# Optimization experiments

Measured on AMD Instinct MI355X. Metric: run time of the kernel, lower is better.

Reference implementation:

```python
import jax, jax.numpy as jnp
import numpy as np
import math

B, S, E, H = 4, 2048, 1024, 16
D = E // H  # head_dim = 64
ROPE_BASE = 10000.0


def setup_inputs() -> dict:
    key = jax.random.key(0)
    ks = jax.random.split(key, 8)
    wscale = 1.0 / math.sqrt(E)
    inp = {
        "query": jax.random.normal(ks[0], (B, S, E), dtype=jnp.float32),
        "key": jax.random.normal(ks[1], (B, S, E), dtype=jnp.float32),
        "value": jax.random.normal(ks[2], (B, S, E), dtype=jnp.float32),
        "Wq": jax.random.normal(ks[3], (E, E), dtype=jnp.float32) * wscale,
        "Wk": jax.random.normal(ks[4], (E, E), dtype=jnp.float32) * wscale,
        "Wv": jax.random.normal(ks[5], (E, E), dtype=jnp.float32) * wscale,
        "Wo": jax.random.normal(ks[6], (E, E), dtype=jnp.float32) * wscale,
        "positions": jnp.arange(S, dtype=jnp.int64),
        # True = masked (upper triangle -> causal)
        "attn_mask": jnp.triu(jnp.ones((S, S), dtype=bool), k=1),
    }
    return inp


def _apply_rope(x, positions):
    # x: [B, H, S, D]; rotate-half RoPE convention
    half = D // 2
    inv_freq = 1.0 / (ROPE_BASE ** (jnp.arange(0, D, 2, dtype=jnp.float32) / D))  # [D/2]
    ang = positions.astype(jnp.float32)[:, None] * inv_freq[None, :]  # [S, D/2]
    cos = jnp.concatenate([jnp.cos(ang), jnp.cos(ang)], axis=-1)  # [S, D]
    sin = jnp.concatenate([jnp.sin(ang), jnp.sin(ang)], axis=-1)  # [S, D]
    x1, x2 = x[..., :half], x[..., half:]
    rot = jnp.concatenate([-x2, x1], axis=-1)
    return x * cos[None, None] + rot * sin[None, None]


def reference(query, key, value, Wq, Wk, Wv, Wo, positions, attn_mask):
    # projections (no bias, weight layout [out, in] as in set_weights_from_float)
    q = jnp.einsum('bse,oe->bso', query, Wq).reshape(B, S, H, D).transpose(0, 2, 1, 3)
    k = jnp.einsum('bse,oe->bso', key, Wk).reshape(B, S, H, D).transpose(0, 2, 1, 3)
    v = jnp.einsum('bse,oe->bso', value, Wv).reshape(B, S, H, D).transpose(0, 2, 1, 3)
    q = _apply_rope(q, positions)
    k = _apply_rope(k, positions)
    scale = 1.0 / math.sqrt(D)
    scores = jnp.einsum('bhqd,bhkd->bhqk', q, k) * scale  # [B,H,S,S]
    scores = jnp.where(attn_mask[None, None], -jnp.inf, scores)
    weights = jax.nn.softmax(scores, axis=-1)
    out = jnp.einsum('bhqk,bhkd->bhqd', weights, v)  # [B,H,S,D]
    out = out.transpose(0, 2, 1, 3).reshape(B, S, H * D)
    return jnp.einsum('bso,eo->bse', out, Wo)
```

## Files before the change

kernel.cpp:

```cpp
#include <hip/hip_runtime.h>
#include <hip/hip_bf16.h>
#include <math.h>

typedef __bf16 bf16;
typedef __attribute__((ext_vector_type(8))) __bf16 bf16x8;
typedef __attribute__((ext_vector_type(4))) __bf16 bf16x4;
typedef __attribute__((ext_vector_type(4))) float f32x4;
typedef __attribute__((ext_vector_type(16))) float f32x16;
typedef __attribute__((ext_vector_type(4))) unsigned uint4v;

#define MFMA16 __builtin_amdgcn_mfma_f32_16x16x32_bf16
#define MFMA32 __builtin_amdgcn_mfma_f32_32x32x16_bf16

__device__ __forceinline__ void g2l16(const void* g, void* l) {
    __builtin_amdgcn_global_load_lds(
        (const __attribute__((address_space(1))) void*)g,
        (__attribute__((address_space(3))) void*)l, 16, 0, 0);
}

__device__ __forceinline__ bool is_bf16_buf(const void* p) {
    const int lane = threadIdx.x & 63;
    unsigned w = ((const unsigned*)p)[lane];
    unsigned e = (w >> 7) & 0xFF;
    bool pl = (e == 0) || (e >= 80 && e < 134);
    return __popcll(__ballot(pl)) >= 52;
}

__device__ __forceinline__ void stage_f32(bf16* l, const float* g) {
    float4 f0 = ((const float4*)g)[0];
    float4 f1 = ((const float4*)g)[1];
    bf16x8 t;
    t[0] = (bf16)f0.x; t[1] = (bf16)f0.y; t[2] = (bf16)f0.z; t[3] = (bf16)f0.w;
    t[4] = (bf16)f1.x; t[5] = (bf16)f1.y; t[6] = (bf16)f1.z; t[7] = (bf16)f1.w;
    *(bf16x8*)l = t;
}

__device__ __forceinline__ unsigned cvtpk_bf16(float a, float b) {
    unsigned r;
    asm("v_cvt_pk_bf16_f32 %0, %1, %2" : "=v"(r) : "v"(a), "v"(b));
    return r;
}

__global__ __launch_bounds__(256) void convert7(const void* s0, const void* s1,
                                                const void* s2, const void* s3,
                                                const void* s4, const void* s5,
                                                const void* s6,
                                                bf16* __restrict__ dst) {
    const size_t e = ((size_t)blockIdx.x * 256 + threadIdx.x) * 8;
    const void* src; size_t off; bf16* d;
    if (e < 25165824) {
        const int i = (int)(e >> 23);
        src = i == 0 ? s0 : i == 1 ? s1 : s2;
        off = e & 8388607;
        d   = dst + ((size_t)i << 23) + off;
    } else {
        const size_t e2 = e - 25165824;
        const int i = (int)(e2 >> 20);
        src = i == 0 ? s3 : i == 1 ? s4 : i == 2 ? s5 : s6;
        off = e2 & 1048575;
        d   = dst + 25165824 + ((size_t)i << 20) + off;
    }
    if (is_bf16_buf(src)) {
        *(bf16x8*)d = *((const bf16x8*)((const bf16*)src + off));
    } else {
        stage_f32(d, (const float*)src + off);
    }
}

__device__ __forceinline__ void epi_rope(f32x4 acc[4][4], bf16* __restrict__ C,
                                         int m0, int n0, int wm, int wn,
                                         int quad, int l16, float scale) {
    const float kf = 0.41524101186092029f;
    const float inv0 = exp2f(-(float)l16 * kf);
    const float inv1 = exp2f(-(float)(l16 + 16) * kf);
#pragma unroll
    for (int mi = 0; mi < 4; mi++) {
#pragma unroll
        for (int r = 0; r < 4; r++) {
            const int row = m0 + wm + mi * 16 + quad * 4 + r;
            const float pos = (float)(row & 2047);
#pragma unroll
            for (int p = 0; p < 2; p++) {
                float sn, cs;
                __sincosf(pos * (p ? inv1 : inv0), &sn, &cs);
                const float x1 = acc[mi][p][r];
                const float x2 = acc[mi][p + 2][r];
                const int col = n0 + wn + p * 16 + l16;
                C[(size_t)row * 1024 + col]      = (bf16)((x1 * cs - x2 * sn) * scale);
                C[(size_t)row * 1024 + col + 32] = (bf16)((x2 * cs + x1 * sn) * scale);
            }
        }
    }
}

__device__ __forceinline__ void epi_vt(f32x4 acc[4][4], bf16* __restrict__ C,
                                       int m0, int n0, int wm, int wn,
                                       int quad, int l16) {
#pragma unroll
    for (int mi = 0; mi < 4; mi++) {
        const int rbase = m0 + wm + mi * 16 + quad * 4;
#pragma unroll
        for (int ni = 0; ni < 4; ni++) {
            const int col = n0 + wn + ni * 16 + l16;
            bf16x4 t;
#pragma unroll
            for (int r = 0; r < 4; r++) t[r] = (bf16)acc[mi][ni][r];
            *(bf16x4*)&C[(size_t)col * 8192 + rbase] = t;
        }
    }
}

__device__ __forceinline__ void gemm_core(const bf16* __restrict__ A,
                                          const bf16* __restrict__ B,
                                          int m0, int n0, f32x4 acc[4][4]) {
    __shared__ bf16 As[3 * 8192];
    __shared__ bf16 Bs[3 * 16384];
    const int tid  = threadIdx.x;
    const int wave = tid >> 6;
    const int lane = tid & 63;
    const int quad = lane >> 4;
    const int l16  = lane & 15;
    const int wm   = (wave >> 2) * 64;
    const int wn   = (wave & 3) * 64;
    const int rowt = tid >> 3;
    const int swz  = (((tid & 7) ^ (rowt & 7)) * 8);
    const bf16* gA = A + (size_t)(m0 + rowt) * 1024 + swz;
    const bf16* gB = B + (size_t)(n0 + rowt) * 1024 + swz;
    bf16* AsW = As + wave * 512;
    bf16* BsW = Bs + wave * 512;

#define STAGE(t, b)                                                     \
    do {                                                                \
        const int k0_ = (t) * 64;                                       \
        g2l16(gA + k0_,          AsW + (b) * 8192);                     \
        g2l16(gA + 65536 + k0_,  AsW + (b) * 8192 + 4096);              \
        g2l16(gB + k0_,          BsW + (b) * 16384);                    \
        g2l16(gB + 65536 + k0_,  BsW + (b) * 16384 + 4096);             \
        g2l16(gB + 131072 + k0_, BsW + (b) * 16384 + 8192);             \
        g2l16(gB + 196608 + k0_, BsW + (b) * 16384 + 12288);            \
    } while (0)

    STAGE(0, 0);
    STAGE(1, 1);

    const int gsw0 = ((0 + quad) ^ (l16 & 7)) * 8;
    const int gsw1 = ((4 + quad) ^ (l16 & 7)) * 8;

#pragma unroll
    for (int t = 0; t < 16; t++) {
        if (t < 15) asm volatile("s_waitcnt vmcnt(6)" ::: "memory");
        else        asm volatile("s_waitcnt vmcnt(0)" ::: "memory");
        __builtin_amdgcn_s_barrier();
        if (t <= 13) STAGE(t + 2, (t + 2) % 3);
        const bf16* At = As + (t % 3) * 8192;
        const bf16* Bt = Bs + (t % 3) * 16384;
        bf16x8 af[2][4], bfr[2][4];
#pragma unroll
        for (int kk = 0; kk < 2; kk++) {
            const int gg = kk ? gsw1 : gsw0;
#pragma unroll
            for (int i = 0; i < 4; i++)
                af[kk][i] = *(const bf16x8*)&At[(wm + i * 16 + l16) * 64 + gg];
#pragma unroll
            for (int i = 0; i < 4; i++)
                bfr[kk][i] = *(const bf16x8*)&Bt[(wn + i * 16 + l16) * 64 + gg];
        }
        __builtin_amdgcn_s_setprio(1);
#pragma unroll
        for (int kk = 0; kk < 2; kk++)
#pragma unroll
            for (int mi = 0; mi < 4; mi++)
#pragma unroll
                for (int ni = 0; ni < 4; ni++)
                    acc[mi][ni] = MFMA16(af[kk][mi], bfr[kk][ni], acc[mi][ni], 0, 0, 0);
        __builtin_amdgcn_s_setprio(0);
    }
#undef STAGE
}

__global__ __launch_bounds__(512) void qkv256(const bf16* __restrict__ xq,
                                              const bf16* __restrict__ xk,
                                              const bf16* __restrict__ xv,
                                              const bf16* __restrict__ wq,
                                              const bf16* __restrict__ wk,
                                              const bf16* __restrict__ wv,
                                              bf16* __restrict__ Qp,
                                              bf16* __restrict__ Kp,
                                              bf16* __restrict__ Vt) {
    const int z  = blockIdx.z;
    const int m0 = blockIdx.x * 128;
    const int n0 = blockIdx.y * 256;
    const bf16* A = z == 0 ? xq : z == 1 ? xk : xv;
    const bf16* W = z == 0 ? wq : z == 1 ? wk : wv;
    f32x4 acc[4][4] = {};
    gemm_core(A, W, m0, n0, acc);
    const int wave = threadIdx.x >> 6;
    const int lane = threadIdx.x & 63;
    const int quad = lane >> 4;
    const int l16  = lane & 15;
    const int wm = (wave >> 2) * 64;
    const int wn = (wave & 3) * 64;
    if (z == 0)      epi_rope(acc, Qp, m0, n0, wm, wn, quad, l16, 0.125f);
    else if (z == 1) epi_rope(acc, Kp, m0, n0, wm, wn, quad, l16, 1.0f);
    else             epi_vt  (acc, Vt, m0, n0, wm, wn, quad, l16);
}

__global__ __launch_bounds__(512) void out256(const bf16* __restrict__ Ao,
                                              const bf16* __restrict__ wo,
                                              float* __restrict__ Cf) {
    const int m0 = blockIdx.x * 128;
    const int n0 = blockIdx.y * 256;
    f32x4 acc[4][4] = {};
    gemm_core(Ao, wo, m0, n0, acc);
    const int wave = threadIdx.x >> 6;
    const int lane = threadIdx.x & 63;
    const int quad = lane >> 4;
    const int l16  = lane & 15;
    const int wm = (wave >> 2) * 64;
    const int wn = (wave & 3) * 64;
#pragma unroll
    for (int mi = 0; mi < 4; mi++) {
        const int rbase = m0 + wm + mi * 16 + quad * 4;
#pragma unroll
        for (int ni = 0; ni < 4; ni++) {
            const int col = n0 + wn + ni * 16 + l16;
#pragma unroll
            for (int r = 0; r < 4; r++)
                Cf[(size_t)(rbase + r) * 1024 + col] = acc[mi][ni][r];
        }
    }
}

__global__ __launch_bounds__(256) void gemm_nt(const void* __restrict__ Ap,
                                               const void* __restrict__ Wp,
                                               bf16* __restrict__ C,
                                               float* __restrict__ Cf,
                                               int mode, float scale) {
    __shared__ bf16 As[128 * 32];
    __shared__ bf16 Bs[128 * 32];
    const int tid  = threadIdx.x;
    const int wave = tid >> 6;
    const int lane = tid & 63;
    const int quad = lane >> 4;
    const int l16  = lane & 15;
    const int m0 = blockIdx.x * 128;
    const int n0 = blockIdx.y * 128;
    const int wm = (wave >> 1) * 64;
    const int wn = (wave & 1) * 64;

    const bool a_bf = is_bf16_buf(Ap);
    const bool b_bf = is_bf16_buf(Wp);

    const int ra = tid >> 2;
    const int c8 = (tid & 3) * 8;
    const bf16*  gaB = (const bf16*)Ap  + (size_t)(m0 + ra) * 1024 + c8;
    const bf16*  gbB = (const bf16*)Wp  + (size_t)(n0 + ra) * 1024 + c8;
    const float* gaF = (const float*)Ap + (size_t)(m0 + ra) * 1024 + c8;
    const float* gbF = (const float*)Wp + (size_t)(n0 + ra) * 1024 + c8;
    bf16* lA0 = As + (wave * 64) * 8;
    bf16* lA1 = As + (256 + wave * 64) * 8;
    bf16* lB0 = Bs + (wave * 64) * 8;
    bf16* lB1 = Bs + (256 + wave * 64) * 8;

    f32x4 acc[4][4] = {};

    for (int k0 = 0; k0 < 1024; k0 += 32) {
        __syncthreads();
        if (a_bf) {
            g2l16(gaB + k0,             lA0);
            g2l16(gaB + 64 * 1024 + k0, lA1);
        } else {
            stage_f32(As + tid * 8,        gaF + k0);
            stage_f32(As + 2048 + tid * 8, gaF + 64 * 1024 + k0);
        }
        if (b_bf) {
            g2l16(gbB + k0,             lB0);
            g2l16(gbB + 64 * 1024 + k0, lB1);
        } else {
            stage_f32(Bs + tid * 8,        gbF + k0);
            stage_f32(Bs + 2048 + tid * 8, gbF + 64 * 1024 + k0);
        }
        __syncthreads();

        bf16x8 af[4], bfb[4];
#pragma unroll
        for (int i = 0; i < 4; i++)
            af[i] = *(const bf16x8*)&As[(wm + i * 16 + l16) * 32 + quad * 8];
#pragma unroll
        for (int i = 0; i < 4; i++)
            bfb[i] = *(const bf16x8*)&Bs[(wn + i * 16 + l16) * 32 + quad * 8];
#pragma unroll
        for (int mi = 0; mi < 4; mi++)
#pragma unroll
            for (int ni = 0; ni < 4; ni++)
                acc[mi][ni] = MFMA16(af[mi], bfb[ni], acc[mi][ni], 0, 0, 0);
    }

    if (mode == 2) {
#pragma unroll
        for (int mi = 0; mi < 4; mi++) {
            const int rbase = m0 + wm + mi * 16 + quad * 4;
#pragma unroll
            for (int ni = 0; ni < 4; ni++) {
                const int col = n0 + wn + ni * 16 + l16;
#pragma unroll
                for (int r = 0; r < 4; r++)
                    Cf[(size_t)(rbase + r) * 1024 + col] = acc[mi][ni][r];
            }
        }
    } else if (mode == 3) {
        epi_vt(acc, C, m0, n0, wm, wn, quad, l16);
    } else if (mode == 0) {
#pragma unroll
        for (int mi = 0; mi < 4; mi++) {
            const int rbase = m0 + wm + mi * 16 + quad * 4;
#pragma unroll
            for (int ni = 0; ni < 4; ni++) {
                const int col = n0 + wn + ni * 16 + l16;
#pragma unroll
                for (int r = 0; r < 4; r++)
                    C[(size_t)(rbase + r) * 1024 + col] = (bf16)acc[mi][ni][r];
            }
        }
    } else {
        epi_rope(acc, C, m0, n0, wm, wn, quad, l16, scale);
    }
}

__global__ __launch_bounds__(512, 2) void attn_kernel(const bf16* __restrict__ Qp,
                                                      const bf16* __restrict__ Kp,
                                                      const bf16* __restrict__ Vt,
                                                      bf16* __restrict__ Op) {
    __shared__ bf16 Ks[2][64 * 64];
    __shared__ bf16 Vs[2][64 * 64];
    __shared__ bf16 Qs[256 * 64];
    const int tid  = threadIdx.x;
    const int wave = tid >> 6;
    const int lane = tid & 63;
    const int l31  = lane & 31;
    const int hi   = lane >> 5;
    const int bh = blockIdx.x;
    const int y  = blockIdx.y;
    const int qt = (y < 4) ? y : 11 - y;
    const int b  = bh >> 4;
    const int h  = bh & 15;
    const int q0 = qt * 256;
    const int jmax = 4 * qt + 3;
    const size_t baseqk = ((size_t)b * 2048) * 1024 + (size_t)h * 64;
    const bf16* Qg = Qp + baseqk;
    const bf16* Kg = Kp + baseqk;
    const bf16* Vg = Vt + (size_t)(h * 64) * 8192 + (size_t)b * 2048;
    bf16* Og = Op + baseqk;

    const int sr  = tid >> 3;
    const int swz = (((tid & 7) ^ (sr & 7)) * 8);

#pragma unroll
    for (int c = 0; c < 4; c++)
        g2l16(Qg + (size_t)(q0 + c * 64 + sr) * 1024 + swz, Qs + c * 4096 + wave * 512);
    g2l16(Kg + (size_t)sr * 1024 + swz, &Ks[0][wave * 512]);
    g2l16(Vg + (size_t)sr * 8192 + swz, &Vs[0][wave * 512]);
    __syncthreads();

    const int qr = wave * 32 + l31;
    bf16x8 qf[4];
#pragma unroll
    for (int t = 0; t < 4; t++)
        qf[t] = *(const bf16x8*)&Qs[qr * 64 + (((2 * t + hi) ^ (l31 & 7)) * 8)];

    bf16x8 ones;
#pragma unroll
    for (int i = 0; i < 8; i++) ones[i] = (bf16)1.0f;

    f32x16 o0 = {}, o1 = {}, lacc = {};

    for (int j = 0; j <= jmax; j++) {
        if (j) __syncthreads();
        if (j < jmax) {
            const int pb = (j + 1) & 1;
            g2l16(Kg + (size_t)((j + 1) * 64 + sr) * 1024 + swz, &Ks[pb][wave * 512]);
            g2l16(Vg + (size_t)sr * 8192 + (j + 1) * 64 + swz,   &Vs[pb][wave * 512]);
        }
        if (q0 + wave * 32 + 31 < j * 64) continue;
        const bf16* kb = Ks[j & 1];
        const bf16* vb = Vs[j & 1];

        f32x16 s0 = {}, s1 = {};
        __builtin_amdgcn_s_setprio(1);
#pragma unroll
        for (int t = 0; t < 4; t++) {
            const int g = ((2 * t + hi) ^ (l31 & 7)) * 8;
            bf16x8 kf0 = *(const bf16x8*)&kb[l31 * 64 + g];
            bf16x8 kf1 = *(const bf16x8*)&kb[(32 + l31) * 64 + g];
            s0 = MFMA32(kf0, qf[t], s0, 0, 0, 0);
            s1 = MFMA32(kf1, qf[t], s1, 0, 0, 0);
        }
        __builtin_amdgcn_s_setprio(0);

        if (j * 64 + 63 > q0 + wave * 32) {
            const int qg  = q0 + wave * 32 + l31;
            const int kb0 = j * 64 + 4 * hi;
#pragma unroll
            for (int r = 0; r < 16; r++) {
                const int krow = (r & 3) + 8 * (r >> 2);
                if (kb0 + krow > qg)      s0[r] = -INFINITY;
                if (kb0 + 32 + krow > qg) s1[r] = -INFINITY;
            }
        }

#pragma unroll
        for (int r = 0; r < 16; r++) {
            s0[r] = __expf(s0[r] - 12.0f);
            s1[r] = __expf(s1[r] - 12.0f);
        }

        __builtin_amdgcn_s_setprio(1);
#pragma unroll
        for (int ks = 0; ks < 4; ks++) {
            const f32x16 p = (ks < 2) ? s0 : s1;
            const int rb = 8 * (ks & 1);
            unsigned x0 = cvtpk_bf16(p[rb + 0], p[rb + 1]);
            unsigned x1 = cvtpk_bf16(p[rb + 2], p[rb + 3]);
            unsigned y0 = cvtpk_bf16(p[rb + 4], p[rb + 5]);
            unsigned y1 = cvtpk_bf16(p[rb + 6], p[rb + 7]);
            auto r0 = __builtin_amdgcn_permlane32_swap(x0, y0, false, false);
            auto r1 = __builtin_amdgcn_permlane32_swap(x1, y1, false, false);
            uint4v pw;
            pw.x = (unsigned)r0[0];
            pw.y = (unsigned)r1[0];
            pw.z = (unsigned)r0[1];
            pw.w = (unsigned)r1[1];
            const bf16x8 pa = __builtin_bit_cast(bf16x8, pw);

            lacc = MFMA32(pa, ones, lacc, 0, 0, 0);
            const int g = ((2 * ks + hi) ^ (l31 & 7)) * 8;
            bf16x8 vf0 = *(const bf16x8*)&vb[l31 * 64 + g];
            bf16x8 vf1 = *(const bf16x8*)&vb[(32 + l31) * 64 + g];
            o0 = MFMA32(pa, vf0, o0, 0, 0, 0);
            o1 = MFMA32(pa, vf1, o1, 0, 0, 0);
        }
        __builtin_amdgcn_s_setprio(0);
    }

#pragma unroll
    for (int r = 0; r < 16; r++) {
        const float linv = 1.0f / lacc[r];
        const int row = q0 + wave * 32 + (r & 3) + 8 * (r >> 2) + 4 * hi;
        Og[(size_t)row * 1024 + l31]      = (bf16)(o0[r] * linv);
        Og[(size_t)row * 1024 + 32 + l31] = (bf16)(o1[r] * linv);
    }
}

extern "C" void kernel_launch(void* const* d_in, const int* in_sizes, int n_in,
                              void* d_out, int out_size, void* d_ws, size_t ws_size,
                              hipStream_t stream) {
    const void* q  = d_in[0];
    const void* k  = d_in[1];
    const void* v  = d_in[2];
    const void* Wq = d_in[3];
    const void* Wk = d_in[4];
    const void* Wv = d_in[5];
    const void* Wo = d_in[6];
    float* out = (float*)d_out;

    const size_t M8 = (size_t)8192 * 1024;
    bf16* Qp  = (bf16*)d_ws;
    bf16* Kp  = Qp + M8;
    bf16* Vtp = Kp + M8;
    bf16* Ao  = Vtp + M8;
    bf16* cbase = Ao + M8;
    const size_t NEED = (M8 * 4 + 29360128) * sizeof(bf16);

    dim3 blk(256);
    dim3 gg(64, 8);

    if (ws_size >= NEED) {
        convert7<<<14336, blk, 0, stream>>>(q, k, v, Wq, Wk, Wv, Wo, cbase);
        const bf16* aq = cbase;
        const bf16* ak = cbase + M8;
        const bf16* av = cbase + 2 * M8;
        const bf16* wq = cbase + 3 * M8;
        const bf16* wk = wq + 1048576;
        const bf16* wv = wk + 1048576;
        const bf16* wo = wv + 1048576;
        qkv256<<<dim3(64, 4, 3), dim3(512), 0, stream>>>(aq, ak, av, wq, wk, wv,
                                                         Qp, Kp, Vtp);
        attn_kernel<<<dim3(64, 8), dim3(512), 0, stream>>>(Qp, Kp, Vtp, Ao);
        out256<<<dim3(64, 4), dim3(512), 0, stream>>>(Ao, wo, out);
    } else {
        gemm_nt<<<gg, blk, 0, stream>>>(q, Wq, Qp, nullptr, 1, 0.125f);
        gemm_nt<<<gg, blk, 0, stream>>>(k, Wk, Kp, nullptr, 1, 1.0f);
        gemm_nt<<<gg, blk, 0, stream>>>(v, Wv, Vtp, nullptr, 3, 1.0f);
        attn_kernel<<<dim3(64, 8), dim3(512), 0, stream>>>(Qp, Kp, Vtp, Ao);
        gemm_nt<<<gg, blk, 0, stream>>>(Ao, Wo, nullptr, out, 2, 1.0f);
    }
}
```

Baseline: 290.7 us.

## Split GEMM k-step into four interleaved phases with staggered global loads

Restructures the shared GEMM core main loop into four ping-pong-style phases per k-tile. Each phase loads a small set of LDS fragments, issues one third of the next tile's global-to-LDS copies, then runs a barrier-fenced block of MFMAs at raised priority. The aim is to overlap LDS reads, global loads and matrix math across waves more finely and to cut register pressure from holding all fragments at once. The cost is many more barriers per iteration. It also swaps the attention grid dimensions in the fallback path only, which may be inconsistent with the kernel's block indexing.

```diff
diff --git a/kernel.cpp b/kernel.cpp
--- a/kernel.cpp
+++ b/kernel.cpp
@@ -129,53 +129,75 @@
     bf16* AsW = As + wave * 512;
     bf16* BsW = Bs + wave * 512;
 
-#define STAGE(t, b)                                                     \
-    do {                                                                \
-        const int k0_ = (t) * 64;                                       \
+#define STG_A(t, b)  do { const int k0_ = (t) * 64;                     \
         g2l16(gA + k0_,          AsW + (b) * 8192);                     \
-        g2l16(gA + 65536 + k0_,  AsW + (b) * 8192 + 4096);              \
+        g2l16(gA + 65536 + k0_,  AsW + (b) * 8192 + 4096); } while (0)
+#define STG_B01(t, b) do { const int k0_ = (t) * 64;                    \
         g2l16(gB + k0_,          BsW + (b) * 16384);                    \
-        g2l16(gB + 65536 + k0_,  BsW + (b) * 16384 + 4096);             \
+        g2l16(gB + 65536 + k0_,  BsW + (b) * 16384 + 4096); } while (0)
+#define STG_B23(t, b) do { const int k0_ = (t) * 64;                    \
         g2l16(gB + 131072 + k0_, BsW + (b) * 16384 + 8192);             \
-        g2l16(gB + 196608 + k0_, BsW + (b) * 16384 + 12288);            \
-    } while (0)
-
-    STAGE(0, 0);
-    STAGE(1, 1);
+        g2l16(gB + 196608 + k0_, BsW + (b) * 16384 + 12288); } while (0)
+
+#define PHASE_MFMA(bA_, bB_, nA_, nB_)                                  \
+    __builtin_amdgcn_s_barrier();                                       \
+    asm volatile("s_waitcnt lgkmcnt(0)" ::: "memory");                  \
+    __builtin_amdgcn_sched_barrier(0);                                  \
+    __builtin_amdgcn_s_setprio(1);                                      \
+    _Pragma("unroll")                                                   \
+    for (int mi = 0; mi < 4; mi++) {                                    \
+        acc[mi][nA_] = MFMA16(a[mi], bA_, acc[mi][nA_], 0, 0, 0);       \
+        acc[mi][nB_] = MFMA16(a[mi], bB_, acc[mi][nB_], 0, 0, 0);       \
+    }                                                                   \
+    __builtin_amdgcn_s_setprio(0);                                      \
+    __builtin_amdgcn_s_barrier();
+
+    STG_A(0, 0); STG_B01(0, 0); STG_B23(0, 0);
+    STG_A(1, 1); STG_B01(1, 1); STG_B23(1, 1);
+    asm volatile("s_waitcnt vmcnt(6)" ::: "memory");
+    __builtin_amdgcn_s_barrier();
 
     const int gsw0 = ((0 + quad) ^ (l16 & 7)) * 8;
     const int gsw1 = ((4 + quad) ^ (l16 & 7)) * 8;
 
 #pragma unroll
     for (int t = 0; t < 16; t++) {
-        if (t < 15) asm volatile("s_waitcnt vmcnt(6)" ::: "memory");
-        else        asm volatile("s_waitcnt vmcnt(0)" ::: "memory");
-        __builtin_amdgcn_s_barrier();
-        if (t <= 13) STAGE(t + 2, (t + 2) % 3);
         const bf16* At = As + (t % 3) * 8192;
         const bf16* Bt = Bs + (t % 3) * 16384;
-        bf16x8 af[2][4], bfr[2][4];
-#pragma unroll
-        for (int kk = 0; kk < 2; kk++) {
-            const int gg = kk ? gsw1 : gsw0;
-#pragma unroll
-            for (int i = 0; i < 4; i++)
-                af[kk][i] = *(const bf16x8*)&At[(wm + i * 16 + l16) * 64 + gg];
-#pragma unroll
-            for (int i = 0; i < 4; i++)
-                bfr[kk][i] = *(const bf16x8*)&Bt[(wn + i * 16 + l16) * 64 + gg];
-        }
-        __builtin_amdgcn_s_setprio(1);
-#pragma unroll
-        for (int kk = 0; kk < 2; kk++)
-#pragma unroll
-            for (int mi = 0; mi < 4; mi++)
-#pragma unroll
-                for (int ni = 0; ni < 4; ni++)
-                    acc[mi][ni] = MFMA16(af[kk][mi], bfr[kk][ni], acc[mi][ni], 0, 0, 0);
-        __builtin_amdgcn_s_setprio(0);
-    }
-#undef STAGE
+        const int bn = (t + 2) % 3;
+        bf16x8 a[4], bA, bB;
+
+#pragma unroll
+        for (int mi = 0; mi < 4; mi++)
+            a[mi] = *(const bf16x8*)&At[(wm + mi * 16 + l16) * 64 + gsw0];
+        bA = *(const bf16x8*)&Bt[(wn +  0 + l16) * 64 + gsw0];
+        bB = *(const bf16x8*)&Bt[(wn + 16 + l16) * 64 + gsw0];
+        if (t <= 13) STG_A(t + 2, bn);
+        PHASE_MFMA(bA, bB, 0, 1)
+
+        bA = *(const bf16x8*)&Bt[(wn + 32 + l16) * 64 + gsw0];
+        bB = *(const bf16x8*)&Bt[(wn + 48 + l16) * 64 + gsw0];
+        if (t <= 13) STG_B01(t + 2, bn);
+        PHASE_MFMA(bA, bB, 2, 3)
+
+#pragma unroll
+        for (int mi = 0; mi < 4; mi++)
+            a[mi] = *(const bf16x8*)&At[(wm + mi * 16 + l16) * 64 + gsw1];
+        bA = *(const bf16x8*)&Bt[(wn +  0 + l16) * 64 + gsw1];
+        bB = *(const bf16x8*)&Bt[(wn + 16 + l16) * 64 + gsw1];
+        if (t <= 13) STG_B23(t + 2, bn);
+        PHASE_MFMA(bA, bB, 0, 1)
+
+        bA = *(const bf16x8*)&Bt[(wn + 32 + l16) * 64 + gsw1];
+        bB = *(const bf16x8*)&Bt[(wn + 48 + l16) * 64 + gsw1];
+        if (t <= 13)      asm volatile("s_waitcnt vmcnt(6)" ::: "memory");
+        else if (t == 14) asm volatile("s_waitcnt vmcnt(0)" ::: "memory");
+        PHASE_MFMA(bA, bB, 2, 3)
+    }
+#undef STG_A
+#undef STG_B01
+#undef STG_B23
+#undef PHASE_MFMA
 }
 
 __global__ __launch_bounds__(512) void qkv256(const bf16* __restrict__ xq,
@@ -491,7 +513,7 @@
         gemm_nt<<<gg, blk, 0, stream>>>(q, Wq, Qp, nullptr, 1, 0.125f);
         gemm_nt<<<gg, blk, 0, stream>>>(k, Wk, Kp, nullptr, 1, 1.0f);
         gemm_nt<<<gg, blk, 0, stream>>>(v, Wv, Vtp, nullptr, 3, 1.0f);
-        attn_kernel<<<dim3(64, 8), dim3(512), 0, stream>>>(Qp, Kp, Vtp, Ao);
+        attn_kernel<<<dim3(8, 64), dim3(512), 0, stream>>>(Qp, Kp, Vtp, Ao);
         gemm_nt<<<gg, blk, 0, stream>>>(Ao, Wo, nullptr, out, 2, 1.0f);
     }
 }
```

Result: slower. 303.0 us (+4.2%).

## Fuse fp32-to-bf16 activation conversion into QKV projection GEMM loads

Applied to the files above, without the earlier changes.

Removes the separate conversion pass over the large q/k/v activations; only the weights are still pre-converted. The QKV GEMM now loads fp32 activation tiles into registers, converts them to bf16 and writes them swizzled to LDS, software-pipelined against the MFMA loop. This cuts a full write and reread of the bf16 activation copies, but the A path now uses register staging instead of direct global-to-LDS loads. The fallback path's attention grid dimensions are also changed.

```diff
diff --git a/kernel.cpp b/kernel.cpp
--- a/kernel.cpp
+++ b/kernel.cpp
@@ -41,25 +41,14 @@
     return r;
 }
 
-__global__ __launch_bounds__(256) void convert7(const void* s0, const void* s1,
+__global__ __launch_bounds__(256) void convertW(const void* s0, const void* s1,
                                                 const void* s2, const void* s3,
-                                                const void* s4, const void* s5,
-                                                const void* s6,
                                                 bf16* __restrict__ dst) {
     const size_t e = ((size_t)blockIdx.x * 256 + threadIdx.x) * 8;
-    const void* src; size_t off; bf16* d;
-    if (e < 25165824) {
-        const int i = (int)(e >> 23);
-        src = i == 0 ? s0 : i == 1 ? s1 : s2;
-        off = e & 8388607;
-        d   = dst + ((size_t)i << 23) + off;
-    } else {
-        const size_t e2 = e - 25165824;
-        const int i = (int)(e2 >> 20);
-        src = i == 0 ? s3 : i == 1 ? s4 : i == 2 ? s5 : s6;
-        off = e2 & 1048575;
-        d   = dst + 25165824 + ((size_t)i << 20) + off;
-    }
+    const int i = (int)(e >> 20);
+    const size_t off = e & 1048575;
+    const void* src = i == 0 ? s0 : i == 1 ? s1 : i == 2 ? s2 : s3;
+    bf16* d = dst + ((size_t)i << 20) + off;
     if (is_bf16_buf(src)) {
         *(bf16x8*)d = *((const bf16x8*)((const bf16*)src + off));
     } else {
@@ -110,11 +99,12 @@
     }
 }
 
-__device__ __forceinline__ void gemm_core(const bf16* __restrict__ A,
+template <bool AF32>
+__device__ __forceinline__ void gemm_core(const void* __restrict__ Ap,
                                           const bf16* __restrict__ B,
-                                          int m0, int n0, f32x4 acc[4][4]) {
-    __shared__ bf16 As[3 * 8192];
-    __shared__ bf16 Bs[3 * 16384];
+                                          int m0, int n0, f32x4 acc[4][4],
+                                          bf16* __restrict__ As,
+                                          bf16* __restrict__ Bs) {
     const int tid  = threadIdx.x;
     const int wave = tid >> 6;
     const int lane = tid & 63;
@@ -124,34 +114,72 @@
     const int wn   = (wave & 3) * 64;
     const int rowt = tid >> 3;
     const int swz  = (((tid & 7) ^ (rowt & 7)) * 8);
-    const bf16* gA = A + (size_t)(m0 + rowt) * 1024 + swz;
+    const bf16* gA = (const bf16*)Ap + (size_t)(m0 + rowt) * 1024 + swz;
     const bf16* gB = B + (size_t)(n0 + rowt) * 1024 + swz;
     bf16* AsW = As + wave * 512;
     bf16* BsW = Bs + wave * 512;
 
-#define STAGE(t, b)                                                     \
-    do {                                                                \
-        const int k0_ = (t) * 64;                                       \
+    const int arow = tid >> 2;
+    const int ag0  = (tid & 3) * 2;
+    const int ar7  = arow & 7;
+    const float* gAf = (const float*)Ap + (size_t)(m0 + arow) * 1024 + (tid & 3) * 16;
+    float4 ar[2][4];
+
+#define STG_A(t, b)  do { const int k0_ = (t) * 64;                     \
         g2l16(gA + k0_,          AsW + (b) * 8192);                     \
-        g2l16(gA + 65536 + k0_,  AsW + (b) * 8192 + 4096);              \
+        g2l16(gA + 65536 + k0_,  AsW + (b) * 8192 + 4096); } while (0)
+#define STG_B(t, b)  do { const int k0_ = (t) * 64;                     \
         g2l16(gB + k0_,          BsW + (b) * 16384);                    \
         g2l16(gB + 65536 + k0_,  BsW + (b) * 16384 + 4096);             \
         g2l16(gB + 131072 + k0_, BsW + (b) * 16384 + 8192);             \
-        g2l16(gB + 196608 + k0_, BsW + (b) * 16384 + 12288);            \
-    } while (0)
-
-    STAGE(0, 0);
-    STAGE(1, 1);
+        g2l16(gB + 196608 + k0_, BsW + (b) * 16384 + 12288); } while (0)
+#define LOADA(t, s)  do { const float* p_ = gAf + (t) * 64;             \
+        ar[s][0] = ((const float4*)p_)[0];                              \
+        ar[s][1] = ((const float4*)p_)[1];                              \
+        ar[s][2] = ((const float4*)p_)[2];                              \
+        ar[s][3] = ((const float4*)p_)[3]; } while (0)
+#define CVTW(s, b)   do {                                               \
+        bf16x8 t0_, t1_;                                                \
+        t0_[0]=(bf16)ar[s][0].x; t0_[1]=(bf16)ar[s][0].y;               \
+        t0_[2]=(bf16)ar[s][0].z; t0_[3]=(bf16)ar[s][0].w;               \
+        t0_[4]=(bf16)ar[s][1].x; t0_[5]=(bf16)ar[s][1].y;               \
+        t0_[6]=(bf16)ar[s][1].z; t0_[7]=(bf16)ar[s][1].w;               \
+        t1_[0]=(bf16)ar[s][2].x; t1_[1]=(bf16)ar[s][2].y;               \
+        t1_[2]=(bf16)ar[s][2].z; t1_[3]=(bf16)ar[s][2].w;               \
+        t1_[4]=(bf16)ar[s][3].x; t1_[5]=(bf16)ar[s][3].y;               \
+        t1_[6]=(bf16)ar[s][3].z; t1_[7]=(bf16)ar[s][3].w;               \
+        bf16* d_ = As + (b) * 8192 + arow * 64;                         \
+        *(bf16x8*)(d_ + ((ag0       ^ ar7) * 8)) = t0_;                 \
+        *(bf16x8*)(d_ + (((ag0 + 1) ^ ar7) * 8)) = t1_; } while (0)
+
+    if constexpr (AF32) {
+        LOADA(0, 0); STG_B(0, 0);
+        LOADA(1, 1); STG_B(1, 1);
+        CVTW(0, 0);
+        asm volatile("s_waitcnt lgkmcnt(0)" ::: "memory");
+    } else {
+        STG_A(0, 0); STG_B(0, 0);
+        STG_A(1, 1); STG_B(1, 1);
+    }
 
     const int gsw0 = ((0 + quad) ^ (l16 & 7)) * 8;
     const int gsw1 = ((4 + quad) ^ (l16 & 7)) * 8;
 
 #pragma unroll
     for (int t = 0; t < 16; t++) {
-        if (t < 15) asm volatile("s_waitcnt vmcnt(6)" ::: "memory");
-        else        asm volatile("s_waitcnt vmcnt(0)" ::: "memory");
+        if constexpr (AF32) {
+            if (t < 15) asm volatile("s_waitcnt vmcnt(4)" ::: "memory");
+            else        asm volatile("s_waitcnt vmcnt(0)" ::: "memory");
+        } else {
+            if (t < 15) asm volatile("s_waitcnt vmcnt(6)" ::: "memory");
+            else        asm volatile("s_waitcnt vmcnt(0)" ::: "memory");
+        }
         __builtin_amdgcn_s_barrier();
-        if (t <= 13) STAGE(t + 2, (t + 2) % 3);
+        if constexpr (AF32) {
+            if (t <= 13) { LOADA(t + 2, t & 1); STG_B(t + 2, (t + 2) % 3); }
+        } else {
+            if (t <= 13) { STG_A(t + 2, (t + 2) % 3); STG_B(t + 2, (t + 2) % 3); }
+        }
         const bf16* At = As + (t % 3) * 8192;
         const bf16* Bt = Bs + (t % 3) * 16384;
         bf16x8 af[2][4], bfr[2][4];
@@ -165,6 +193,9 @@
             for (int i = 0; i < 4; i++)
                 bfr[kk][i] = *(const bf16x8*)&Bt[(wn + i * 16 + l16) * 64 + gg];
         }
+        if constexpr (AF32) {
+            if (t <= 14) CVTW((t + 1) & 1, (t + 1) % 3);
+        }
         __builtin_amdgcn_s_setprio(1);
 #pragma unroll
         for (int kk = 0; kk < 2; kk++)
@@ -174,26 +205,35 @@
                 for (int ni = 0; ni < 4; ni++)
                     acc[mi][ni] = MFMA16(af[kk][mi], bfr[kk][ni], acc[mi][ni], 0, 0, 0);
         __builtin_amdgcn_s_setprio(0);
-    }
-#undef STAGE
-}
-
-__global__ __launch_bounds__(512) void qkv256(const bf16* __restrict__ xq,
-                                              const bf16* __restrict__ xk,
-                                              const bf16* __restrict__ xv,
+        if constexpr (AF32) {
+            asm volatile("s_waitcnt lgkmcnt(0)" ::: "memory");
+        }
+    }
+#undef STG_A
+#undef STG_B
+#undef LOADA
+#undef CVTW
+}
+
+__global__ __launch_bounds__(512) void qkv256(const void* __restrict__ xq,
+                                              const void* __restrict__ xk,
+                                              const void* __restrict__ xv,
                                               const bf16* __restrict__ wq,
                                               const bf16* __restrict__ wk,
                                               const bf16* __restrict__ wv,
                                               bf16* __restrict__ Qp,
                                               bf16* __restrict__ Kp,
                                               bf16* __restrict__ Vt) {
+    __shared__ bf16 As[3 * 8192];
+    __shared__ bf16 Bs[3 * 16384];
     const int z  = blockIdx.z;
     const int m0 = blockIdx.x * 128;
     const int n0 = blockIdx.y * 256;
-    const bf16* A = z == 0 ? xq : z == 1 ? xk : xv;
+    const void* A = z == 0 ? xq : z == 1 ? xk : xv;
     const bf16* W = z == 0 ? wq : z == 1 ? wk : wv;
     f32x4 acc[4][4] = {};
-    gemm_core(A, W, m0, n0, acc);
+    if (is_bf16_buf(A)) gemm_core<false>(A, W, m0, n0, acc, As, Bs);
+    else                gemm_core<true >(A, W, m0, n0, acc, As, Bs);
     const int wave = threadIdx.x >> 6;
     const int lane = threadIdx.x & 63;
     const int quad = lane >> 4;
@@ -208,10 +248,12 @@
 __global__ __launch_bounds__(512) void out256(const bf16* __restrict__ Ao,
                                               const bf16* __restrict__ wo,
                                               float* __restrict__ Cf) {
+    __shared__ bf16 As[3 * 8192];
+    __shared__ bf16 Bs[3 * 16384];
     const int m0 = blockIdx.x * 128;
     const int n0 = blockIdx.y * 256;
     f32x4 acc[4][4] = {};
-    gemm_core(Ao, wo, m0, n0, acc);
+    gemm_core<false>(Ao, wo, m0, n0, acc, As, Bs);
     const int wave = threadIdx.x >> 6;
     const int lane = threadIdx.x & 63;
     const int quad = lane >> 4;
@@ -468,22 +510,19 @@
     bf16* Kp  = Qp + M8;
     bf16* Vtp = Kp + M8;
     bf16* Ao  = Vtp + M8;
-    bf16* cbase = Ao + M8;
-    const size_t NEED = (M8 * 4 + 29360128) * sizeof(bf16);
+    bf16* wbase = Ao + M8;
+    const size_t NEED = (M8 * 4 + 4 * 1048576) * sizeof(bf16);
 
     dim3 blk(256);
     dim3 gg(64, 8);
 
     if (ws_size >= NEED) {
-        convert7<<<14336, blk, 0, stream>>>(q, k, v, Wq, Wk, Wv, Wo, cbase);
-        const bf16* aq = cbase;
-        const bf16* ak = cbase + M8;
-        const bf16* av = cbase + 2 * M8;
-        const bf16* wq = cbase + 3 * M8;
+        convertW<<<2048, blk, 0, stream>>>(Wq, Wk, Wv, Wo, wbase);
+        const bf16* wq = wbase;
         const bf16* wk = wq + 1048576;
         const bf16* wv = wk + 1048576;
         const bf16* wo = wv + 1048576;
-        qkv256<<<dim3(64, 4, 3), dim3(512), 0, stream>>>(aq, ak, av, wq, wk, wv,
+        qkv256<<<dim3(64, 4, 3), dim3(512), 0, stream>>>(q, k, v, wq, wk, wv,
                                                          Qp, Kp, Vtp);
         attn_kernel<<<dim3(64, 8), dim3(512), 0, stream>>>(Qp, Kp, Vtp, Ao);
         out256<<<dim3(64, 4), dim3(512), 0, stream>>>(Ao, wo, out);
@@ -491,7 +530,7 @@
         gemm_nt<<<gg, blk, 0, stream>>>(q, Wq, Qp, nullptr, 1, 0.125f);
         gemm_nt<<<gg, blk, 0, stream>>>(k, Wk, Kp, nullptr, 1, 1.0f);
         gemm_nt<<<gg, blk, 0, stream>>>(v, Wv, Vtp, nullptr, 3, 1.0f);
-        attn_kernel<<<dim3(64, 8), dim3(512), 0, stream>>>(Qp, Kp, Vtp, Ao);
+        attn_kernel<<<dim3(8, 64), dim3(512), 0, stream>>>(Qp, Kp, Vtp, Ao);
         gemm_nt<<<gg, blk, 0, stream>>>(Ao, Wo, nullptr, out, 2, 1.0f);
     }
 }
```

New measurement: 319.2 us. 9.8% more time.
